# Kernel tuning notes

Hardware: AMD Instinct MI355X
Metric: run time of the kernel (lower is better)

## Reference

```python
import jax, jax.numpy as jnp
import numpy as np

M, K, N, G = 64, 4096, 11008, 128  # tokens, infeatures, outfeatures, group_size
NUM_GROUPS = K // G  # 32


def _fp8_round_trip(w):
    # Simulate FP8 E4M3 storage of the quantized weight codes.
    return w.astype(jnp.float8_e4m3fn).astype(jnp.float32)


def setup_inputs() -> dict:
    key = jax.random.key(0)
    k1, k2, k3, k4 = jax.random.split(key, 4)
    x = jax.random.normal(k1, (M, K), dtype=jnp.float32)
    # FP8-representable weight codes (post round-trip, stored as f32 values)
    weight = _fp8_round_trip(jax.random.normal(k2, (N, K), dtype=jnp.float32) * 2.0)
    # Per-(out_feature, group) dequant scales, strictly positive
    weight_scale = jax.random.uniform(k3, (N, NUM_GROUPS), dtype=jnp.float32,
                                      minval=0.005, maxval=0.02)
    bias = jax.random.normal(k4, (N,), dtype=jnp.float32)
    return {"x": x, "weight": weight, "weight_scale": weight_scale, "bias": bias}


def reference(x, weight, weight_scale, bias):
    # Dequantize: each group of `G` consecutive in-features of an output row
    # shares one scale -> w_deq[o, i] = weight[o, i] * scale[o, i // G]
    n, k = weight.shape
    g = k // weight_scale.shape[1]
    w_deq = (weight.reshape(n, -1, g) * weight_scale[:, :, None]).reshape(n, k)
    # Fused dequant-matmul: out[m, o] = sum_i x[m, i] * w_deq[o, i] + bias[o]
    out = jnp.einsum("mk,nk->mn", x, w_deq) + bias
    return out
```

## Files before the change

### kernel.cpp

```cpp
#include <hip/hip_runtime.h>


#define Md 64
#define Kd 4096
#define Nd 11008
#define NGROUPS 32
#define BK 128
#define BN 64
#define KSPLIT 4
#define KCHUNK (Kd / KSPLIT)
#define NITER (KCHUNK / BK)
#define LDSS (BK + 8)

typedef __attribute__((ext_vector_type(8))) __bf16 bf16x8;
typedef __attribute__((ext_vector_type(4))) __bf16 bf16x4;
typedef __attribute__((ext_vector_type(4))) float f32x4;

__global__ __launch_bounds__(256, 4)
void qlinear_pass1(const float* __restrict__ x,
                   const float* __restrict__ w,
                   const float* __restrict__ scale,
                   float* __restrict__ ws)
{
    const int tid  = threadIdx.x;
    const int wv   = tid >> 6;
    const int lane = tid & 63;
    const int quad = lane >> 4;
    const int ln   = lane & 15;

    const int n0 = blockIdx.x * BN;
    const int ky = blockIdx.y;
    const int k0 = ky * KCHUNK;

    const int col4 = tid & 31;
    const int row0 = tid >> 5;
    const float* wsrc = w + (size_t)(n0 + row0) * Kd + k0 + col4 * 4;
    const float* xsrc = x + (size_t)row0 * Kd + k0 + col4 * 4;

    __shared__ __bf16 lds_w[BN * LDSS];
    __shared__ __bf16 lds_x[Md * LDSS];

    const int ng = n0 + wv * 16 + ln;
    float sc[8];
    {
        const float* sp = scale + (size_t)ng * NGROUPS + ky * NITER;
        float4 s0 = *(const float4*)(sp);
        float4 s1 = *(const float4*)(sp + 4);
        sc[0]=s0.x; sc[1]=s0.y; sc[2]=s0.z; sc[3]=s0.w;
        sc[4]=s1.x; sc[5]=s1.y; sc[6]=s1.z; sc[7]=s1.w;
    }

    f32x4 acc[4];
    #pragma unroll
    for (int t = 0; t < 4; ++t) acc[t] = (f32x4){0.f, 0.f, 0.f, 0.f};

    float4 wreg[8], xreg[8];
    #pragma unroll
    for (int j = 0; j < 8; ++j) {
        wreg[j] = *(const float4*)(wsrc + (size_t)(8 * j) * Kd);
        xreg[j] = *(const float4*)(xsrc + (size_t)(8 * j) * Kd);
    }

    for (int i = 0; i < NITER; ++i) {
        #pragma unroll
        for (int j = 0; j < 8; ++j) {
            const int off = (row0 + 8 * j) * LDSS + col4 * 4;
            float4 v = wreg[j];
            *(bf16x4*)&lds_w[off] =
                (bf16x4){(__bf16)v.x, (__bf16)v.y, (__bf16)v.z, (__bf16)v.w};
            float4 u = xreg[j];
            *(bf16x4*)&lds_x[off] =
                (bf16x4){(__bf16)u.x, (__bf16)u.y, (__bf16)u.z, (__bf16)u.w};
        }
        __syncthreads();

        if (i + 1 < NITER) {
            const float* wp = wsrc + (i + 1) * BK;
            const float* xp = xsrc + (i + 1) * BK;
            #pragma unroll
            for (int j = 0; j < 8; ++j) {
                wreg[j] = *(const float4*)(wp + (size_t)(8 * j) * Kd);
                xreg[j] = *(const float4*)(xp + (size_t)(8 * j) * Kd);
            }
        }

        f32x4 pg[4];
        #pragma unroll
        for (int t = 0; t < 4; ++t) pg[t] = (f32x4){0.f, 0.f, 0.f, 0.f};

        #pragma unroll
        for (int ks = 0; ks < 4; ++ks) {
            const int ko = ks * 32 + quad * 8;
            bf16x8 wf = *(const bf16x8*)&lds_w[(wv * 16 + ln) * LDSS + ko];
            #pragma unroll
            for (int t = 0; t < 4; ++t) {
                bf16x8 xf = *(const bf16x8*)&lds_x[(t * 16 + ln) * LDSS + ko];
                pg[t] = __builtin_amdgcn_mfma_f32_16x16x32_bf16(xf, wf, pg[t],
                                                                0, 0, 0);
            }
        }

        const float s = sc[i];
        #pragma unroll
        for (int t = 0; t < 4; ++t)
            #pragma unroll
            for (int r = 0; r < 4; ++r)
                acc[t][r] += s * pg[t][r];

        __syncthreads();
    }

    float* wp = ws + ((size_t)ky * Md) * Nd + n0 + wv * 16 + ln;
    #pragma unroll
    for (int t = 0; t < 4; ++t)
        #pragma unroll
        for (int r = 0; r < 4; ++r)
            wp[(size_t)(t * 16 + quad * 4 + r) * Nd] = acc[t][r];
}

__global__ __launch_bounds__(256)
void qlinear_reduce(const float* __restrict__ ws,
                    const float* __restrict__ bias,
                    float* __restrict__ out)
{
    const int idx = blockIdx.x * 256 + threadIdx.x;
    if (idx >= Md * Nd) return;
    const int n = idx % Nd;
    float v = bias[n];
    #pragma unroll
    for (int ky = 0; ky < KSPLIT; ++ky)
        v += ws[(size_t)ky * Md * Nd + idx];
    out[idx] = v;
}

extern "C" void kernel_launch(void* const* d_in, const int* in_sizes, int n_in,
                              void* d_out, int out_size, void* d_ws, size_t ws_size,
                              hipStream_t stream) {
    const float* x     = (const float*)d_in[0];
    const float* w     = (const float*)d_in[1];
    const float* scale = (const float*)d_in[2];
    const float* bias  = (const float*)d_in[3];
    float* out = (float*)d_out;
    float* ws  = (float*)d_ws;

    dim3 grid1(Nd / BN, KSPLIT);
    qlinear_pass1<<<grid1, 256, 0, stream>>>(x, w, scale, ws);

    const int total = Md * Nd;
    qlinear_reduce<<<(total + 255) / 256, 256, 0, stream>>>(ws, bias, out);
}
```

Measured before the change: 291.9 us.

## Load weight fragments directly into registers, skipping LDS staging, and double the K split

```diff
diff --git a/kernel.cpp b/kernel.cpp
--- a/kernel.cpp
+++ b/kernel.cpp
@@ -5,15 +5,15 @@
 #define Kd 4096
 #define Nd 11008
 #define NGROUPS 32
-#define BK 128
 #define BN 64
-#define KSPLIT 4
+#define BK 64
+#define KSPLIT 8
 #define KCHUNK (Kd / KSPLIT)
 #define NITER (KCHUNK / BK)
-#define LDSS (BK + 8)
+#define NGRP (KCHUNK / 128)
+#define XLD (BK + 8)
 
 typedef __attribute__((ext_vector_type(8))) __bf16 bf16x8;
-typedef __attribute__((ext_vector_type(4))) __bf16 bf16x4;
 typedef __attribute__((ext_vector_type(4))) float f32x4;
 
 __global__ __launch_bounds__(256, 4)
@@ -32,90 +32,92 @@
     const int ky = blockIdx.y;
     const int k0 = ky * KCHUNK;
 
-    const int col4 = tid & 31;
-    const int row0 = tid >> 5;
-    const float* wsrc = w + (size_t)(n0 + row0) * Kd + k0 + col4 * 4;
-    const float* xsrc = x + (size_t)row0 * Kd + k0 + col4 * 4;
+    const int nrow = n0 + wv * 16 + ln;
+    const float* wp = w + (size_t)nrow * Kd + k0 + quad * 8;
 
-    __shared__ __bf16 lds_w[BN * LDSS];
-    __shared__ __bf16 lds_x[Md * LDSS];
+    const int xrow = tid >> 2;
+    const int xc0  = (tid & 3) * 16;
+    const float* xp = x + (size_t)xrow * Kd + k0 + xc0;
 
-    const int ng = n0 + wv * 16 + ln;
-    float sc[8];
-    {
-        const float* sp = scale + (size_t)ng * NGROUPS + ky * NITER;
-        float4 s0 = *(const float4*)(sp);
-        float4 s1 = *(const float4*)(sp + 4);
-        sc[0]=s0.x; sc[1]=s0.y; sc[2]=s0.z; sc[3]=s0.w;
-        sc[4]=s1.x; sc[5]=s1.y; sc[6]=s1.z; sc[7]=s1.w;
-    }
+    __shared__ __bf16 lds_x[Md * XLD];
+
+    float4 sc4 = *(const float4*)(scale + (size_t)nrow * NGROUPS + ky * NGRP);
+    const float sc[4] = {sc4.x, sc4.y, sc4.z, sc4.w};
 
     f32x4 acc[4];
     #pragma unroll
     for (int t = 0; t < 4; ++t) acc[t] = (f32x4){0.f, 0.f, 0.f, 0.f};
 
-    float4 wreg[8], xreg[8];
+    float4 wreg[2][4], xreg[2][4];
     #pragma unroll
-    for (int j = 0; j < 8; ++j) {
-        wreg[j] = *(const float4*)(wsrc + (size_t)(8 * j) * Kd);
-        xreg[j] = *(const float4*)(xsrc + (size_t)(8 * j) * Kd);
-    }
+    for (int j = 0; j < 4; ++j)
+        xreg[0][j] = *(const float4*)(xp + j * 4);
+    wreg[0][0] = *(const float4*)(wp + 0);
+    wreg[0][1] = *(const float4*)(wp + 4);
+    wreg[0][2] = *(const float4*)(wp + 32);
+    wreg[0][3] = *(const float4*)(wp + 36);
 
-    for (int i = 0; i < NITER; ++i) {
-        #pragma unroll
-        for (int j = 0; j < 8; ++j) {
-            const int off = (row0 + 8 * j) * LDSS + col4 * 4;
-            float4 v = wreg[j];
-            *(bf16x4*)&lds_w[off] =
-                (bf16x4){(__bf16)v.x, (__bf16)v.y, (__bf16)v.z, (__bf16)v.w};
-            float4 u = xreg[j];
-            *(bf16x4*)&lds_x[off] =
-                (bf16x4){(__bf16)u.x, (__bf16)u.y, (__bf16)u.z, (__bf16)u.w};
-        }
-        __syncthreads();
-
-        if (i + 1 < NITER) {
-            const float* wp = wsrc + (i + 1) * BK;
-            const float* xp = xsrc + (i + 1) * BK;
-            #pragma unroll
-            for (int j = 0; j < 8; ++j) {
-                wreg[j] = *(const float4*)(wp + (size_t)(8 * j) * Kd);
-                xreg[j] = *(const float4*)(xp + (size_t)(8 * j) * Kd);
-            }
-        }
-
+    #pragma unroll
+    for (int g = 0; g < NGRP; ++g) {
         f32x4 pg[4];
         #pragma unroll
         for (int t = 0; t < 4; ++t) pg[t] = (f32x4){0.f, 0.f, 0.f, 0.f};
 
         #pragma unroll
-        for (int ks = 0; ks < 4; ++ks) {
-            const int ko = ks * 32 + quad * 8;
-            bf16x8 wf = *(const bf16x8*)&lds_w[(wv * 16 + ln) * LDSS + ko];
+        for (int sub = 0; sub < 2; ++sub) {
+            const int i   = g * 2 + sub;
+            const int buf = i & 1;
+
             #pragma unroll
-            for (int t = 0; t < 4; ++t) {
-                bf16x8 xf = *(const bf16x8*)&lds_x[(t * 16 + ln) * LDSS + ko];
-                pg[t] = __builtin_amdgcn_mfma_f32_16x16x32_bf16(xf, wf, pg[t],
-                                                                0, 0, 0);
+            for (int j = 0; j < 2; ++j) {
+                float4 a = xreg[buf][2 * j], b = xreg[buf][2 * j + 1];
+                bf16x8 v = {(__bf16)a.x, (__bf16)a.y, (__bf16)a.z, (__bf16)a.w,
+                            (__bf16)b.x, (__bf16)b.y, (__bf16)b.z, (__bf16)b.w};
+                *(bf16x8*)&lds_x[xrow * XLD + xc0 + j * 8] = v;
             }
+            __syncthreads();
+
+            if (i + 1 < NITER) {
+                const int nb = buf ^ 1;
+                #pragma unroll
+                for (int j = 0; j < 4; ++j)
+                    xreg[nb][j] = *(const float4*)(xp + (i + 1) * BK + j * 4);
+                wreg[nb][0] = *(const float4*)(wp + (i + 1) * BK + 0);
+                wreg[nb][1] = *(const float4*)(wp + (i + 1) * BK + 4);
+                wreg[nb][2] = *(const float4*)(wp + (i + 1) * BK + 32);
+                wreg[nb][3] = *(const float4*)(wp + (i + 1) * BK + 36);
+            }
+
+            #pragma unroll
+            for (int ks = 0; ks < 2; ++ks) {
+                float4 wa = wreg[buf][2 * ks], wb = wreg[buf][2 * ks + 1];
+                bf16x8 wf = {(__bf16)wa.x, (__bf16)wa.y, (__bf16)wa.z, (__bf16)wa.w,
+                             (__bf16)wb.x, (__bf16)wb.y, (__bf16)wb.z, (__bf16)wb.w};
+                #pragma unroll
+                for (int t = 0; t < 4; ++t) {
+                    bf16x8 xf = *(const bf16x8*)
+                        &lds_x[(t * 16 + ln) * XLD + ks * 32 + quad * 8];
+                    pg[t] = __builtin_amdgcn_mfma_f32_16x16x32_bf16(xf, wf, pg[t],
+                                                                    0, 0, 0);
+                }
+            }
+            __syncthreads();
         }
 
-        const float s = sc[i];
+        const float s = sc[g];
         #pragma unroll
         for (int t = 0; t < 4; ++t)
             #pragma unroll
             for (int r = 0; r < 4; ++r)
                 acc[t][r] += s * pg[t][r];
-
-        __syncthreads();
     }
 
-    float* wp = ws + ((size_t)ky * Md) * Nd + n0 + wv * 16 + ln;
+    float* op = ws + ((size_t)ky * Md) * Nd + n0 + wv * 16 + ln;
     #pragma unroll
     for (int t = 0; t < 4; ++t)
         #pragma unroll
         for (int r = 0; r < 4; ++r)
-            wp[(size_t)(t * 16 + quad * 4 + r) * Nd] = acc[t][r];
+            op[(size_t)(t * 16 + quad * 4 + r) * Nd] = acc[t][r];
 }
 
 __global__ __launch_bounds__(256)
```

Measured after the change: 274.8 us. 5.8% less time.
